# Optimization experiments

Measured on AMD Instinct MI355X. Metric: run time of the kernel, lower is better.

## Reference

```python
import jax, jax.numpy as jnp
import numpy as np

NUM_CLASSES = 100000
NUM_FEATURES = 256
BATCH = 1024
MOMENTUM = 0.5
SCALAR = 30.0
EPS = 1e-12  # matches F.normalize eps


def _l2norm(x, axis=-1):
    n = jnp.linalg.norm(x, axis=axis, keepdims=True)
    return x / jnp.maximum(n, EPS)


def setup_inputs() -> dict:
    key = jax.random.key(0)
    k1, k2, k3 = jax.random.split(key, 3)
    inputs = jax.random.normal(k1, (BATCH, NUM_FEATURES), dtype=jnp.float32)
    targets = jax.random.randint(k2, (BATCH,), 0, NUM_CLASSES, dtype=jnp.int32)
    # OIM memory bank buffer (non-trainable); random instead of zeros to avoid 0/0 in normalize
    weight = jax.random.normal(k3, (NUM_CLASSES, NUM_FEATURES), dtype=jnp.float32)
    return {"inputs": inputs, "targets": targets, "weight": weight}


def reference(inputs, targets, weight):
    # l2_norm=True path
    x = _l2norm(inputs, axis=1)          # [B, D]
    w = _l2norm(weight, axis=1)          # [C, D]
    predicts = (x @ w.T) * SCALAR        # [B, C]

    # Sequential per-sample momentum update of the (raw) memory bank, as in the
    # torch for-loop: weight[y] = normalize(m*weight[y] + (1-m)*x_normalized)
    def step(wbuf, xy):
        xi, yi = xy
        row = MOMENTUM * wbuf[yi] + (1.0 - MOMENTUM) * xi
        row = row / jnp.maximum(jnp.linalg.norm(row), EPS)
        return wbuf.at[yi].set(row), None

    new_weight, _ = jax.lax.scan(step, weight, (x, targets))
    return predicts, targets, new_weight
```

## Files before the change

### kernel.cpp

```cpp
#include <hip/hip_runtime.h>

#define NUM_CLASSES 100000
#define NUM_FEATURES 256
#define BATCH 1024
#define SCALARF 30.0f
#define EPSF 1e-12f

typedef __attribute__((ext_vector_type(4))) float float4v;
typedef __attribute__((ext_vector_type(8))) short short8;
typedef __attribute__((ext_vector_type(4))) short short4v;

static __device__ inline short f2bf(float f) {
    unsigned u = __builtin_bit_cast(unsigned, f);
    unsigned r = (u + 0x7FFFu + ((u >> 16) & 1u)) >> 16;
    return (short)r;
}

static __device__ inline float wave_reduce_sum(float s) {
#pragma unroll
    for (int off = 32; off > 0; off >>= 1) s += __shfl_xor(s, off, 64);
    return s;
}

__global__ __launch_bounds__(64) void xnorm_kernel(const float* __restrict__ x,
                                                   const int* __restrict__ tgt,
                                                   float* __restrict__ xn,
                                                   short* __restrict__ xnb,
                                                   float* __restrict__ out_tgt) {
    int row = blockIdx.x;
    int lane = threadIdx.x;
    const float4v v = *(const float4v*)(x + (size_t)row * NUM_FEATURES + lane * 4);
    float s = v.x * v.x + v.y * v.y + v.z * v.z + v.w * v.w;
    s = wave_reduce_sum(s);
    float scale = 1.0f / fmaxf(sqrtf(s), EPSF);
    float4v nv = v * scale;
    *(float4v*)(xn + (size_t)row * NUM_FEATURES + lane * 4) = nv;
    short4v bv;
    bv.x = f2bf(nv.x); bv.y = f2bf(nv.y); bv.z = f2bf(nv.z); bv.w = f2bf(nv.w);
    *(short4v*)(xnb + (size_t)row * NUM_FEATURES + lane * 4) = bv;
    if (lane == 0) out_tgt[row] = (float)tgt[row];
}

__global__ __launch_bounds__(256) void wnorm_kernel(const float* __restrict__ w,
                                                    short* __restrict__ wnb,
                                                    float* __restrict__ out_w) {
    int row = blockIdx.x * 4 + (threadIdx.x >> 6);
    int lane = threadIdx.x & 63;
    const float4v v = *(const float4v*)(w + (size_t)row * NUM_FEATURES + lane * 4);
    float s = v.x * v.x + v.y * v.y + v.z * v.z + v.w * v.w;
    s = wave_reduce_sum(s);
    float scale = 1.0f / fmaxf(sqrtf(s), EPSF);
    *(float4v*)(out_w + (size_t)row * NUM_FEATURES + lane * 4) = v;
    float4v nv = v * scale;
    short4v bv;
    bv.x = f2bf(nv.x); bv.y = f2bf(nv.y); bv.z = f2bf(nv.z); bv.w = f2bf(nv.w);
    *(short4v*)(wnb + (size_t)row * NUM_FEATURES + lane * 4) = bv;
}

__global__ __launch_bounds__(1024) void chain_kernel(const int* __restrict__ tgt,
                                                     int* __restrict__ head,
                                                     int* __restrict__ nxt) {
    __shared__ int t[BATCH];
    int i = threadIdx.x;
    t[i] = tgt[i];
    __syncthreads();
    int mine = t[i];
    int h = 1;
    for (int j = 0; j < i; ++j)
        if (t[j] == mine) { h = 0; break; }
    int nx = -1;
    for (int j = i + 1; j < BATCH; ++j)
        if (t[j] == mine) { nx = j; break; }
    head[i] = h;
    nxt[i] = nx;
}

__global__ __launch_bounds__(64) void update_kernel(const float* __restrict__ xn,
                                                    const float* __restrict__ w_raw,
                                                    const int* __restrict__ tgt,
                                                    const int* __restrict__ head,
                                                    const int* __restrict__ nxt,
                                                    float* __restrict__ out_w) {
    int i = blockIdx.x;
    if (!head[i]) return;
    int lane = threadIdx.x;
    int t = tgt[i];
    float4v row = *(const float4v*)(w_raw + (size_t)t * NUM_FEATURES + lane * 4);
    int cur = i;
    while (cur >= 0) {
        const float4v xv = *(const float4v*)(xn + (size_t)cur * NUM_FEATURES + lane * 4);
        row = row * 0.5f + xv * 0.5f;
        float s = row.x * row.x + row.y * row.y + row.z * row.z + row.w * row.w;
        s = wave_reduce_sum(s);
        float scale = 1.0f / fmaxf(sqrtf(s), EPSF);
        row = row * scale;
        cur = nxt[cur];
    }
    *(float4v*)(out_w + (size_t)t * NUM_FEATURES + lane * 4) = row;
}

__global__ __launch_bounds__(256) void gemm_kernel(const short* __restrict__ xnb,
                                                   const short* __restrict__ wnb,
                                                   float* __restrict__ out) {
    int tid = threadIdx.x;
    int lane = tid & 63;
    int wave = tid >> 6;
    int wm = wave & 1;
    int wn = wave >> 1;
    int m0 = blockIdx.x * 128 + wm * 64;
    int n0 = blockIdx.y * 128 + wn * 64;
    int r16 = lane & 15;
    int quad = lane >> 4;

    float4v acc[4][4];
#pragma unroll
    for (int i = 0; i < 4; ++i)
#pragma unroll
        for (int j = 0; j < 4; ++j) acc[i][j] = (float4v){0.f, 0.f, 0.f, 0.f};

    int nrow[4];
#pragma unroll
    for (int j = 0; j < 4; ++j) {
        int n = n0 + j * 16 + r16;
        nrow[j] = n < NUM_CLASSES ? n : (NUM_CLASSES - 1);
    }
    int arow[4];
#pragma unroll
    for (int i = 0; i < 4; ++i) arow[i] = m0 + i * 16 + r16;

    for (int s = 0; s < 8; ++s) {
        int k0 = s * 32 + quad * 8;
        short8 a[4], b[4];
#pragma unroll
        for (int i = 0; i < 4; ++i)
            a[i] = *(const short8*)(xnb + (size_t)arow[i] * NUM_FEATURES + k0);
#pragma unroll
        for (int j = 0; j < 4; ++j)
            b[j] = *(const short8*)(wnb + (size_t)nrow[j] * NUM_FEATURES + k0);
#pragma unroll
        for (int i = 0; i < 4; ++i)
#pragma unroll
            for (int j = 0; j < 4; ++j)
                acc[i][j] = __builtin_amdgcn_mfma_f32_16x16x32_bf16(a[i], b[j], acc[i][j], 0, 0, 0);
    }

#pragma unroll
    for (int i = 0; i < 4; ++i) {
#pragma unroll
        for (int j = 0; j < 4; ++j) {
            int n = n0 + j * 16 + r16;
            if (n < NUM_CLASSES) {
#pragma unroll
                for (int r = 0; r < 4; ++r) {
                    int m = m0 + i * 16 + quad * 4 + r;
                    out[(size_t)m * NUM_CLASSES + n] = acc[i][j][r] * SCALARF;
                }
            }
        }
    }
}

extern "C" void kernel_launch(void* const* d_in, const int* in_sizes, int n_in,
                              void* d_out, int out_size, void* d_ws, size_t ws_size,
                              hipStream_t stream) {
    const float* x = (const float*)d_in[0];
    const int* tgt = (const int*)d_in[1];
    const float* w = (const float*)d_in[2];

    float* out = (float*)d_out;
    float* out_pred = out;
    float* out_tgt = out + (size_t)BATCH * NUM_CLASSES;
    float* out_w = out_tgt + BATCH;

    char* ws = (char*)d_ws;
    float* xn = (float*)ws;
    short* xnb = (short*)(ws + (1 << 20));
    short* wnb = (short*)(ws + (1 << 20) + (1 << 19));
    int* head = (int*)(ws + (1 << 20) + (1 << 19) + (size_t)NUM_CLASSES * NUM_FEATURES * 2);
    int* nxt = head + BATCH;

    xnorm_kernel<<<BATCH, 64, 0, stream>>>(x, tgt, xn, xnb, out_tgt);
    wnorm_kernel<<<NUM_CLASSES / 4, 256, 0, stream>>>(w, wnb, out_w);
    chain_kernel<<<1, BATCH, 0, stream>>>(tgt, head, nxt);
    update_kernel<<<BATCH, 64, 0, stream>>>(xn, w, tgt, head, nxt, out_w);
    dim3 grid(BATCH / 128, (NUM_CLASSES + 127) / 128);
    gemm_kernel<<<grid, 256, 0, stream>>>(xnb, wnb, out_pred);
}
```

Baseline: 814.7 us.

## Fuse duplicate-chain detection into update kernel and vectorize GEMM output stores

Removes the separate single-block chain kernel and has each update block find duplicates and next occurrences itself, using shared memory and wave ballots. The GEMM swaps the MFMA operand order so each lane holds four consecutive output columns, which allows 16-byte vector stores instead of scalar stores. It also double-buffers the register loads across K steps and remaps block IDs on a 1D grid so neighbouring blocks share weight tiles. The main target is the 400MB prediction write, with the rest trimming launch overhead and load latency.

```diff
diff --git a/kernel.cpp b/kernel.cpp
--- a/kernel.cpp
+++ b/kernel.cpp
@@ -57,35 +57,22 @@
     *(short4v*)(wnb + (size_t)row * NUM_FEATURES + lane * 4) = bv;
 }
 
-__global__ __launch_bounds__(1024) void chain_kernel(const int* __restrict__ tgt,
-                                                     int* __restrict__ head,
-                                                     int* __restrict__ nxt) {
-    __shared__ int t[BATCH];
-    int i = threadIdx.x;
-    t[i] = tgt[i];
-    __syncthreads();
-    int mine = t[i];
-    int h = 1;
-    for (int j = 0; j < i; ++j)
-        if (t[j] == mine) { h = 0; break; }
-    int nx = -1;
-    for (int j = i + 1; j < BATCH; ++j)
-        if (t[j] == mine) { nx = j; break; }
-    head[i] = h;
-    nxt[i] = nx;
-}
-
 __global__ __launch_bounds__(64) void update_kernel(const float* __restrict__ xn,
                                                     const float* __restrict__ w_raw,
                                                     const int* __restrict__ tgt,
-                                                    const int* __restrict__ head,
-                                                    const int* __restrict__ nxt,
                                                     float* __restrict__ out_w) {
+    __shared__ int t[BATCH];
     int i = blockIdx.x;
-    if (!head[i]) return;
     int lane = threadIdx.x;
-    int t = tgt[i];
-    float4v row = *(const float4v*)(w_raw + (size_t)t * NUM_FEATURES + lane * 4);
+    for (int j = lane; j < BATCH; j += 64) t[j] = tgt[j];
+    __syncthreads();
+    int mine = t[i];
+    bool dup = false;
+    for (int j = lane; j < i; j += 64)
+        if (t[j] == mine) { dup = true; break; }
+    if (__any(dup)) return;
+
+    float4v row = *(const float4v*)(w_raw + (size_t)mine * NUM_FEATURES + lane * 4);
     int cur = i;
     while (cur >= 0) {
         const float4v xv = *(const float4v*)(xn + (size_t)cur * NUM_FEATURES + lane * 4);
@@ -94,21 +81,35 @@
         s = wave_reduce_sum(s);
         float scale = 1.0f / fmaxf(sqrtf(s), EPSF);
         row = row * scale;
-        cur = nxt[cur];
+        int nx = -1;
+        for (int base = cur + 1; base < BATCH; base += 64) {
+            int j = base + lane;
+            bool m = (j < BATCH) && (t[j] == mine);
+            unsigned long long mask = __ballot(m);
+            if (mask) { nx = base + (int)__builtin_ctzll(mask); break; }
+        }
+        cur = nx;
     }
-    *(float4v*)(out_w + (size_t)t * NUM_FEATURES + lane * 4) = row;
+    *(float4v*)(out_w + (size_t)mine * NUM_FEATURES + lane * 4) = row;
 }
 
+#define GRID_MX 8
+#define GRID_NY 782
 __global__ __launch_bounds__(256) void gemm_kernel(const short* __restrict__ xnb,
                                                    const short* __restrict__ wnb,
                                                    float* __restrict__ out) {
+    int id = blockIdx.x;
+    int orig = (id & 7) * (GRID_MX * GRID_NY / 8) + (id >> 3);
+    int bx = orig & 7;
+    int by = orig >> 3;
+
     int tid = threadIdx.x;
     int lane = tid & 63;
     int wave = tid >> 6;
     int wm = wave & 1;
     int wn = wave >> 1;
-    int m0 = blockIdx.x * 128 + wm * 64;
-    int n0 = blockIdx.y * 128 + wn * 64;
+    int m0 = bx * 128 + wm * 64;
+    int n0 = by * 128 + wn * 64;
     int r16 = lane & 15;
     int quad = lane >> 4;
 
@@ -118,43 +119,55 @@
 #pragma unroll
         for (int j = 0; j < 4; ++j) acc[i][j] = (float4v){0.f, 0.f, 0.f, 0.f};
 
-    int nrow[4];
+    const short* abase[4];
+    const short* bbase[4];
+#pragma unroll
+    for (int i = 0; i < 4; ++i) {
+        int m = m0 + i * 16 + r16;
+        abase[i] = xnb + (size_t)m * NUM_FEATURES + quad * 8;
+    }
 #pragma unroll
     for (int j = 0; j < 4; ++j) {
         int n = n0 + j * 16 + r16;
-        nrow[j] = n < NUM_CLASSES ? n : (NUM_CLASSES - 1);
+        n = n < NUM_CLASSES ? n : (NUM_CLASSES - 1);
+        bbase[j] = wnb + (size_t)n * NUM_FEATURES + quad * 8;
     }
-    int arow[4];
+
+    short8 a[2][4], b[2][4];
 #pragma unroll
-    for (int i = 0; i < 4; ++i) arow[i] = m0 + i * 16 + r16;
+    for (int i = 0; i < 4; ++i) a[0][i] = *(const short8*)(abase[i]);
+#pragma unroll
+    for (int j = 0; j < 4; ++j) b[0][j] = *(const short8*)(bbase[j]);
 
+#pragma unroll
     for (int s = 0; s < 8; ++s) {
-        int k0 = s * 32 + quad * 8;
-        short8 a[4], b[4];
+        const int cur = s & 1;
+        const int nxt = cur ^ 1;
+        if (s < 7) {
+            const int k0 = (s + 1) * 32;
 #pragma unroll
-        for (int i = 0; i < 4; ++i)
-            a[i] = *(const short8*)(xnb + (size_t)arow[i] * NUM_FEATURES + k0);
+            for (int i = 0; i < 4; ++i) a[nxt][i] = *(const short8*)(abase[i] + k0);
 #pragma unroll
-        for (int j = 0; j < 4; ++j)
-            b[j] = *(const short8*)(wnb + (size_t)nrow[j] * NUM_FEATURES + k0);
+            for (int j = 0; j < 4; ++j) b[nxt][j] = *(const short8*)(bbase[j] + k0);
+        }
 #pragma unroll
         for (int i = 0; i < 4; ++i)
 #pragma unroll
             for (int j = 0; j < 4; ++j)
-                acc[i][j] = __builtin_amdgcn_mfma_f32_16x16x32_bf16(a[i], b[j], acc[i][j], 0, 0, 0);
+                acc[i][j] = __builtin_amdgcn_mfma_f32_16x16x32_bf16(b[cur][j], a[cur][i],
+                                                                    acc[i][j], 0, 0, 0);
     }
 
 #pragma unroll
-    for (int i = 0; i < 4; ++i) {
+    for (int j = 0; j < 4; ++j) {
+        int nb = n0 + j * 16;
+        if (nb < NUM_CLASSES) {
+            int n = nb + quad * 4;
 #pragma unroll
-        for (int j = 0; j < 4; ++j) {
-            int n = n0 + j * 16 + r16;
-            if (n < NUM_CLASSES) {
-#pragma unroll
-                for (int r = 0; r < 4; ++r) {
-                    int m = m0 + i * 16 + quad * 4 + r;
-                    out[(size_t)m * NUM_CLASSES + n] = acc[i][j][r] * SCALARF;
-                }
+            for (int i = 0; i < 4; ++i) {
+                int m = m0 + i * 16 + r16;
+                float4v v = acc[i][j] * SCALARF;
+                *(float4v*)(out + (size_t)m * NUM_CLASSES + n) = v;
             }
         }
     }
@@ -176,13 +189,9 @@
     float* xn = (float*)ws;
     short* xnb = (short*)(ws + (1 << 20));
     short* wnb = (short*)(ws + (1 << 20) + (1 << 19));
-    int* head = (int*)(ws + (1 << 20) + (1 << 19) + (size_t)NUM_CLASSES * NUM_FEATURES * 2);
-    int* nxt = head + BATCH;
 
     xnorm_kernel<<<BATCH, 64, 0, stream>>>(x, tgt, xn, xnb, out_tgt);
     wnorm_kernel<<<NUM_CLASSES / 4, 256, 0, stream>>>(w, wnb, out_w);
-    chain_kernel<<<1, BATCH, 0, stream>>>(tgt, head, nxt);
-    update_kernel<<<BATCH, 64, 0, stream>>>(xn, w, tgt, head, nxt, out_w);
-    dim3 grid(BATCH / 128, (NUM_CLASSES + 127) / 128);
-    gemm_kernel<<<grid, 256, 0, stream>>>(xnb, wnb, out_pred);
+    update_kernel<<<BATCH, 64, 0, stream>>>(xn, w, tgt, out_w);
+    gemm_kernel<<<GRID_MX * GRID_NY, 256, 0, stream>>>(xnb, wnb, out_pred);
 }
```

After: 774.4 us. 4.9% less time.
